# Performance work log

Hardware: AMD Instinct MI355X
Metric: run time of the kernel (lower is better)

The kernel has to match this reference:

```python
import jax, jax.numpy as jnp
from jax import lax
import numpy as np

N = 20000        # nodes
E = 160000       # directed edges (doubled to 2E inside forward)
NODE_DIM = 6
EDGE_DIM = 4
HID = 64         # hidden_dim
HEADS = 4
ITERS = 3
D_OUT = HEADS * HID          # 256
SQRT_D = 8.0                 # sqrt(HID)
ALLOWED = jnp.array([8., 23., 39., 54., 90., 180.], dtype=jnp.float32)


def _ln(x, g, b):
    m = jnp.mean(x, -1, keepdims=True)
    v = jnp.mean((x - m) ** 2, -1, keepdims=True)
    return (x - m) * lax.rsqrt(v + 1e-5) * g + b


def _cbam(x, w1, b1, w2, b2, cw, cb):
    # channel attention: pool over nodes (dim 0)
    pool = jnp.concatenate([x.max(0, keepdims=True), x.mean(0, keepdims=True)], axis=1)  # [1,2D]
    ch = jax.nn.sigmoid(jnp.maximum(pool @ w1 + b1, 0.) @ w2 + b2)                        # [1,D]
    x = x * ch
    # spatial attention: pool over features, conv1d over node axis
    cat = jnp.concatenate([x.max(-1, keepdims=True), x.mean(-1, keepdims=True)], axis=-1)  # [N,2]
    inp = cat.T[None]                                                                       # [1,2,N]
    sp = lax.conv_general_dilated(inp, cw, (1,), [(3, 3)],
                                  dimension_numbers=('NCH', 'OIH', 'NCH')) + cb[None, :, None]
    return x * jax.nn.sigmoid(sp)[0, 0][:, None]


def _tconv(xc, src, dst, wq, b_q, wk, b_k, wv, b_v, ws, b_s):
    # PyG TransformerConv (concat=True, root_weight=True, no edge features)
    n = xc.shape[0]
    q = (xc @ wq + b_q).reshape(n, HEADS, HID)
    k = (xc @ wk + b_k).reshape(n, HEADS, HID)
    v = (xc @ wv + b_v).reshape(n, HEADS, HID)
    alpha = jnp.einsum('ehd,ehd->eh', q[dst], k[src]) / SQRT_D           # [2E,H]
    amax = jax.ops.segment_max(alpha, dst, num_segments=n)
    a = jnp.exp(alpha - amax[dst])
    a = a / jax.ops.segment_sum(a, dst, num_segments=n)[dst]
    out = jax.ops.segment_sum(a[..., None] * v[src], dst, num_segments=n).reshape(n, D_OUT)
    return out + xc @ ws + b_s


def reference(x, edge_attr, node_w, node_b, edge_w, edge_b, z_emb,
              cn_w1, cn_b1, cn_w2, cn_b2, cn_cw, cn_cb,
              ce_w1, ce_b1, ce_w2, ce_b2, ce_cw, ce_cb,
              Wq, bq, Wk, bk, Wv, bv, Ws, bs,
              lt_g, lt_b, lc_g, lc_b,
              pe_w, pe_b, pn_w, pn_b, gf_w, gf_b,
              c_w1, c_b1, c_w2, c_b2, edge_index):
    send = jnp.concatenate([edge_index[0], edge_index[1]])
    recv = jnp.concatenate([edge_index[1], edge_index[0]])
    src, dst = send, recv                                           # [2E]
    rel = x[src, :3] - x[dst, :3]                                   # [2E,3]
    zi = jnp.argmin(jnp.abs(jnp.round(x[:, 2])[:, None] - ALLOWED[None, :]), axis=1)
    nf = jnp.maximum(x @ node_w + node_b, 0.) + z_emb[zi]           # node embedding + z embedding
    nf = _cbam(nf, cn_w1, cn_b1, cn_w2, cn_b2, cn_cw, cn_cb)
    ef = jnp.concatenate([jnp.concatenate([edge_attr, edge_attr], 0), rel], axis=1)
    ef = jnp.maximum(ef @ edge_w + edge_b, 0.)
    ef = _cbam(ef, ce_w1, ce_b1, ce_w2, ce_b2, ce_cw, ce_cb)
    n = nf.shape[0]
    for i in range(ITERS):
        x0, e0 = nf, ef
        agg = jax.ops.segment_sum(ef, dst, num_segments=n)          # scatter-add messages
        comb = _ln(jnp.concatenate([nf, agg - nf], 1), lc_g[i], lc_b[i])
        out = _tconv(comb, src, dst, Wq[i], bq[i], Wk[i], bk[i], Wv[i], bv[i], Ws[i], bs[i])
        out = _ln(out, lt_g[i], lt_b[i])
        pn = out @ pn_w[i] + pn_b[i]
        g = jax.nn.sigmoid(jnp.concatenate([nf, pn], 1) @ gf_w[i] + gf_b[i])  # gated fusion
        nf = nf * g + pn * (1. - g)
        ef = (out[src] - out[dst]) @ pe_w[i] + pe_b[i]
        nf = nf + x0
        ef = ef + e0
    clf = jnp.concatenate([nf[edge_index[0]], nf[edge_index[1]]], axis=1)
    h = jnp.maximum(clf @ c_w1 + c_b1, 0.)
    return (h @ c_w2 + c_b2)[:, 0]


def setup_inputs() -> dict:
    key = jax.random.key(0)
    ki = iter(jax.random.split(key, 64))
    def rn(shape, s=0.05):
        return jax.random.normal(next(ki), shape, dtype=jnp.float32) * s
    x = jax.random.normal(next(ki), (N, NODE_DIM), dtype=jnp.float32)
    x = x.at[:, 2].set(ALLOWED[jax.random.randint(next(ki), (N,), 0, 6)])
    inp = {
        'x': x,
        'edge_attr': jax.random.normal(next(ki), (E, EDGE_DIM), dtype=jnp.float32),
        'node_w': rn((NODE_DIM, HID)), 'node_b': jnp.zeros(HID),
        'edge_w': rn((EDGE_DIM + 3, HID)), 'edge_b': jnp.zeros(HID),
        'z_emb': rn((6, HID)),
        'cn_w1': rn((2 * HID, HID // 16)), 'cn_b1': jnp.zeros(HID // 16),
        'cn_w2': rn((HID // 16, HID)), 'cn_b2': jnp.zeros(HID),
        'cn_cw': rn((1, 2, 7)), 'cn_cb': jnp.zeros(1),
        'ce_w1': rn((2 * HID, HID // 16)), 'ce_b1': jnp.zeros(HID // 16),
        'ce_w2': rn((HID // 16, HID)), 'ce_b2': jnp.zeros(HID),
        'ce_cw': rn((1, 2, 7)), 'ce_cb': jnp.zeros(1),
        'Wq': rn((ITERS, 2 * HID, D_OUT)), 'bq': jnp.zeros((ITERS, D_OUT)),
        'Wk': rn((ITERS, 2 * HID, D_OUT)), 'bk': jnp.zeros((ITERS, D_OUT)),
        'Wv': rn((ITERS, 2 * HID, D_OUT)), 'bv': jnp.zeros((ITERS, D_OUT)),
        'Ws': rn((ITERS, 2 * HID, D_OUT)), 'bs': jnp.zeros((ITERS, D_OUT)),
        'lt_g': jnp.ones((ITERS, D_OUT)), 'lt_b': jnp.zeros((ITERS, D_OUT)),
        'lc_g': jnp.ones((ITERS, 2 * HID)), 'lc_b': jnp.zeros((ITERS, 2 * HID)),
        'pe_w': rn((ITERS, D_OUT, HID)), 'pe_b': jnp.zeros((ITERS, HID)),
        'pn_w': rn((ITERS, D_OUT, HID)), 'pn_b': jnp.zeros((ITERS, HID)),
        'gf_w': rn((ITERS, 2 * HID, HID)), 'gf_b': jnp.zeros((ITERS, HID)),
        'c_w1': rn((2 * HID, HID)), 'c_b1': jnp.zeros(HID),
        'c_w2': rn((HID, 1)), 'c_b2': jnp.zeros(1),
        'edge_index': jax.random.randint(next(ki), (2, E), 0, N),
    }
    return inp
```

## Files before the change

kernel.cpp:

```cpp
#include <hip/hip_runtime.h>
#include <math.h>

typedef __attribute__((ext_vector_type(8))) short short8;
typedef __attribute__((ext_vector_type(4))) float f32x4;

__device__ __forceinline__ float wave_sum(float v){
  #pragma unroll
  for (int m = 32; m; m >>= 1) v += __shfl_xor(v, m, 64);
  return v;
}
__device__ __forceinline__ float wave_max(float v){
  #pragma unroll
  for (int m = 32; m; m >>= 1) v = fmaxf(v, __shfl_xor(v, m, 64));
  return v;
}
__device__ __forceinline__ unsigned fenc(float f){
  unsigned u = __float_as_uint(f);
  return (u >> 31) ? ~u : (u | 0x80000000u);
}
__device__ __forceinline__ float fdec(unsigned e){
  return (e >> 31) ? __uint_as_float(e & 0x7fffffffu) : __uint_as_float(~e);
}
__device__ __forceinline__ float sigm(float x){ return 1.f / (1.f + __expf(-x)); }
__device__ __forceinline__ unsigned short f2bf(float f){
  union { float f; unsigned u; } x; x.f = f;
  unsigned r = x.u + 0x7fffu + ((x.u >> 16) & 1u);
  return (unsigned short)(r >> 16);
}
__device__ __forceinline__ float bf2f(unsigned short h){
  union { unsigned u; float f; } x; x.u = ((unsigned)h) << 16;
  return x.f;
}

__global__ void k_build_edges(const int* __restrict__ ei, int E2, int E,
                              int* __restrict__ src, int* __restrict__ dst,
                              int* __restrict__ deg){
  int e = blockIdx.x * blockDim.x + threadIdx.x;
  if (e >= E2) return;
  int s = ei[e];
  int d = (e < E) ? ei[e + E] : ei[e - E];
  src[e] = s; dst[e] = d;
  atomicAdd(&deg[d], 1);
}

__global__ void k_scan(const int* __restrict__ deg, int* __restrict__ rowptr, int N){
  __shared__ int part[1024];
  int t = threadIdx.x;
  int chunk = (N + 1023) / 1024;
  int lo = t * chunk, hi = lo + chunk; if (hi > N) hi = N;
  int s = 0;
  for (int i = lo; i < hi; ++i) s += deg[i];
  part[t] = s;
  __syncthreads();
  for (int off = 1; off < 1024; off <<= 1){
    int v = (t >= off) ? part[t - off] : 0;
    __syncthreads();
    part[t] += v;
    __syncthreads();
  }
  int run = part[t] - s;
  for (int i = lo; i < hi; ++i){ rowptr[i] = run; run += deg[i]; }
  if (t == 1023) rowptr[N] = part[1023];
}

__global__ void k_fill(const int* __restrict__ src, const int* __restrict__ dst,
                       const int* __restrict__ rowptr,
                       int* __restrict__ cur, int* __restrict__ csrc,
                       int* __restrict__ epos,
                       const float* __restrict__ x, const float* __restrict__ ea,
                       float* __restrict__ re8, int E2, int E){
  int e = blockIdx.x * blockDim.x + threadIdx.x;
  if (e >= E2) return;
  int s = src[e], d = dst[e];
  int pos = rowptr[d] + atomicAdd(&cur[d], 1);
  csrc[pos] = s;
  epos[e] = pos;
  int row = (e < E) ? e : e - E;
  float4 eav = *reinterpret_cast<const float4*>(ea + (size_t)row*4);
  float r0 = x[s*6]     - x[d*6];
  float r1 = x[s*6 + 1] - x[d*6 + 1];
  float r2 = x[s*6 + 2] - x[d*6 + 2];
  *reinterpret_cast<float4*>(re8 + (size_t)e*8)     = eav;
  *reinterpret_cast<float4*>(re8 + (size_t)e*8 + 4) = make_float4(r0, r1, r2, 0.f);
}

__global__ void k_embed_pool(const float* __restrict__ x, const float* __restrict__ nw,
                             const float* __restrict__ nb, const float* __restrict__ zemb,
                             float* __restrict__ nf,
                             unsigned* __restrict__ pmax, float* __restrict__ psum, int N){
  int tx = threadIdx.x & 63;
  int ty = threadIdx.x >> 6;
  const float allowed[6] = {8.f, 23.f, 39.f, 54.f, 90.f, 180.f};
  float m = -INFINITY, s = 0.f;
  for (int n = blockIdx.x*4 + ty; n < N; n += gridDim.x*4){
    float xv[6];
    #pragma unroll
    for (int k = 0; k < 6; ++k) xv[k] = x[n*6 + k];
    float v = nb[tx];
    #pragma unroll
    for (int k = 0; k < 6; ++k) v += xv[k] * nw[k*64 + tx];
    v = fmaxf(v, 0.f);
    float r = rintf(xv[2]);
    int zi = 0; float bd = fabsf(r - allowed[0]);
    #pragma unroll
    for (int k = 1; k < 6; ++k){ float d = fabsf(r - allowed[k]); if (d < bd){ bd = d; zi = k; } }
    v += zemb[zi*64 + tx];
    nf[(size_t)n*64 + tx] = v;
    m = fmaxf(m, v); s += v;
  }
  __shared__ float sm[4][64], ss[4][64];
  sm[ty][tx] = m; ss[ty][tx] = s;
  __syncthreads();
  if (ty == 0){
    #pragma unroll
    for (int k = 1; k < 4; ++k){ m = fmaxf(m, sm[k][tx]); s += ss[k][tx]; }
    atomicMax(&pmax[tx], fenc(m));
    atomicAdd(&psum[tx], s);
  }
}

__global__ void k_cbam_mlp(const unsigned* __restrict__ pmax, const float* __restrict__ psum,
                           float invR,
                           const float* __restrict__ w1, const float* __restrict__ b1,
                           const float* __restrict__ w2, const float* __restrict__ b2,
                           float* __restrict__ ch){
  __shared__ float pool[128];
  __shared__ float h[4];
  int t = threadIdx.x;
  pool[t]      = fdec(pmax[t]);
  pool[64 + t] = psum[t] * invR;
  __syncthreads();
  if (t < 4){
    float a = b1[t];
    for (int k = 0; k < 128; ++k) a += pool[k] * w1[k*4 + t];
    h[t] = fmaxf(a, 0.f);
  }
  __syncthreads();
  float a = b2[t];
  #pragma unroll
  for (int k = 0; k < 4; ++k) a += h[k] * w2[k*64 + t];
  ch[t] = sigm(a);
}

__global__ void k_chmul_rowpool(float* __restrict__ buf, const float* __restrict__ ch,
                                float* __restrict__ rp, int R){
  int r = blockIdx.x*4 + (threadIdx.x >> 6);
  if (r >= R) return;
  int l = threadIdx.x & 63;
  float v = buf[(size_t)r*64 + l] * ch[l];
  buf[(size_t)r*64 + l] = v;
  float m = wave_max(v);
  float s = wave_sum(v);
  if (l == 0){ rp[(size_t)r*2] = m; rp[(size_t)r*2 + 1] = s * (1.f/64.f); }
}

__global__ void k_spatial(float* __restrict__ buf, const float* __restrict__ rp,
                          const float* __restrict__ cw, const float* __restrict__ cb, int R){
  int r = blockIdx.x*4 + (threadIdx.x >> 6);
  if (r >= R) return;
  int l = threadIdx.x & 63;
  float sp = cb[0];
  #pragma unroll
  for (int t = 0; t < 7; ++t){
    int rr = r + t - 3;
    if (rr >= 0 && rr < R)
      sp += cw[t] * rp[(size_t)rr*2] + cw[7 + t] * rp[(size_t)rr*2 + 1];
  }
  buf[(size_t)r*64 + l] *= sigm(sp);
}

__global__ __launch_bounds__(256) void k_ecol(
    const float* __restrict__ re8,
    const float* __restrict__ ew, const float* __restrict__ eb,
    unsigned* __restrict__ pmax, float* __restrict__ psum, int E2){
  __shared__ float s_ew[448];
  __shared__ float s_re[256];
  int tid = threadIdx.x;
  for (int idx = tid; idx < 448; idx += 256) s_ew[idx] = ew[idx];
  int tx = tid & 63, wv = tid >> 6;
  float ebl = eb[tx];
  float m = -INFINITY, s = 0.f;
  for (int base = blockIdx.x*32; base < E2; base += gridDim.x*32){
    __syncthreads();
    int gidx = base*8 + tid;
    s_re[tid] = (gidx < E2*8) ? re8[gidx] : 0.f;
    __syncthreads();
    #pragma unroll
    for (int j = 0; j < 8; ++j){
      int e = base + wv*8 + j;
      if (e >= E2) break;
      const float* r = &s_re[(wv*8 + j)*8];
      float v = ebl;
      #pragma unroll
      for (int k = 0; k < 7; ++k) v += r[k] * s_ew[k*64 + tx];
      v = fmaxf(v, 0.f);
      m = fmaxf(m, v); s += v;
    }
  }
  __shared__ float sm[4][64], ss[4][64];
  sm[wv][tx] = m; ss[wv][tx] = s;
  __syncthreads();
  if (wv == 0){
    #pragma unroll
    for (int k = 1; k < 4; ++k){ m = fmaxf(m, sm[k][tx]); s += ss[k][tx]; }
    atomicMax(&pmax[tx], fenc(m));
    atomicAdd(&psum[tx], s);
  }
}

__global__ __launch_bounds__(256) void k_erp2(
    const float* __restrict__ re8, const int* __restrict__ epos,
    const float* __restrict__ ew, const float* __restrict__ eb,
    const float* __restrict__ ch,
    float* __restrict__ rp, float* __restrict__ ef0, int E2){
  __shared__ float s_ew[448];
  __shared__ float s_re[256];
  __shared__ int   s_ep[32];
  int tid = threadIdx.x;
  for (int idx = tid; idx < 448; idx += 256) s_ew[idx] = ew[idx];
  int tx = tid & 63, wv = tid >> 6;
  float ebl = eb[tx], chl = ch[tx];
  for (int base = blockIdx.x*32; base < E2; base += gridDim.x*32){
    __syncthreads();
    int gidx = base*8 + tid;
    s_re[tid] = (gidx < E2*8) ? re8[gidx] : 0.f;
    if (tid < 32 && base + tid < E2) s_ep[tid] = epos[base + tid];
    __syncthreads();
    #pragma unroll
    for (int j = 0; j < 8; ++j){
      int e = base + wv*8 + j;
      if (e >= E2) break;
      const float* r = &s_re[(wv*8 + j)*8];
      float v = ebl;
      #pragma unroll
      for (int k = 0; k < 7; ++k) v += r[k] * s_ew[k*64 + tx];
      v = fmaxf(v, 0.f) * chl;
      float mm = wave_max(v);
      float sm2 = wave_sum(v);
      if (tx == 0){ rp[(size_t)e*2] = mm; rp[(size_t)e*2 + 1] = sm2 * (1.f/64.f); }
      ef0[(size_t)s_ep[wv*8 + j]*64 + tx] = v;
    }
  }
}

__global__ void k_se(const float* __restrict__ rp, const int* __restrict__ epos,
                     const float* __restrict__ ccw, const float* __restrict__ ccb,
                     float* __restrict__ se, int E2){
  int e = blockIdx.x * blockDim.x + threadIdx.x;
  if (e >= E2) return;
  float sp = ccb[0];
  #pragma unroll
  for (int t = 0; t < 7; ++t){
    int rr = e + t - 3;
    if (rr >= 0 && rr < E2)
      sp += ccw[t] * rp[(size_t)rr*2] + ccw[7+t] * rp[(size_t)rr*2 + 1];
  }
  se[epos[e]] = sigm(sp);
}

__global__ void k_aggb(const float* __restrict__ ef0, const float* __restrict__ se,
                       const int* __restrict__ rowptr, const float* __restrict__ nf,
                       const float* __restrict__ g, const float* __restrict__ b,
                       float* __restrict__ agg, unsigned short* __restrict__ comb, int N){
  int n = blockIdx.x*4 + (threadIdx.x >> 6);
  if (n >= N) return;
  int l = threadIdx.x & 63;
  int lo = rowptr[n], hi = rowptr[n+1];
  float acc = 0.f;
  int i = lo;
  for (; i + 4 <= hi; i += 4){
    float s0 = se[i], s1 = se[i+1], s2 = se[i+2], s3 = se[i+3];
    float e0 = ef0[(size_t)i*64 + l];
    float e1 = ef0[(size_t)(i+1)*64 + l];
    float e2 = ef0[(size_t)(i+2)*64 + l];
    float e3 = ef0[(size_t)(i+3)*64 + l];
    acc += s0*e0 + s1*e1 + s2*e2 + s3*e3;
  }
  for (; i < hi; ++i) acc += se[i] * ef0[(size_t)i*64 + l];
  agg[(size_t)n*64 + l] = acc;
  float a = nf[(size_t)n*64 + l];
  float v0 = a, v1 = acc - a;
  float mean = wave_sum(v0 + v1) * (1.f/128.f);
  float d0 = v0 - mean, d1 = v1 - mean;
  float var = wave_sum(d0*d0 + d1*d1) * (1.f/128.f);
  float rs = rsqrtf(var + 1e-5f);
  comb[(size_t)n*128 + l]      = f2bf(d0 * rs * g[l]      + b[l]);
  comb[(size_t)n*128 + 64 + l] = f2bf(d1 * rs * g[64 + l] + b[64 + l]);
}

__global__ __launch_bounds__(256) void k_packT1(
    const float* __restrict__ Wq, const float* __restrict__ Wk,
    const float* __restrict__ Wv, const float* __restrict__ Ws,
    unsigned short* __restrict__ Bt){
  __shared__ float t[64][65];
  int bx = blockIdx.x, by = blockIdx.y, bz = blockIdx.z;
  const float* W = (bz == 0) ? Wq : (bz == 1) ? Wk : (bz == 2) ? Wv : Ws;
  int tx = threadIdx.x & 63, ty = threadIdx.x >> 6;
  int R0 = by*64, C0 = bx*64;
  for (int r = ty; r < 64; r += 4)
    t[r][tx] = W[(size_t)(R0 + r)*256 + C0 + tx];
  __syncthreads();
  int iter = by >> 1, kr0 = (by & 1)*64;
  for (int r = ty; r < 64; r += 4)
    Bt[(size_t)iter*1024*128 + (size_t)(bz*256 + C0 + r)*128 + kr0 + tx] = f2bf(t[tx][r]);
}

__global__ __launch_bounds__(256) void k_packT2(
    const float* __restrict__ Wn, const float* __restrict__ We,
    unsigned short* __restrict__ Bt2){
  __shared__ float t[64][65];
  int by = blockIdx.y, bz = blockIdx.z;
  const float* W = (bz == 0) ? Wn : We;
  int tx = threadIdx.x & 63, ty = threadIdx.x >> 6;
  int R0 = by*64;
  for (int r = ty; r < 64; r += 4)
    t[r][tx] = W[(size_t)(R0 + r)*64 + tx];
  __syncthreads();
  int iter = by >> 2, kr0 = (by & 3)*64;
  for (int r = ty; r < 64; r += 4)
    Bt2[(size_t)iter*128*256 + (size_t)(bz*64 + r)*256 + kr0 + tx] = f2bf(t[tx][r]);
}

__global__ void k_biasp(const float* __restrict__ bq, const float* __restrict__ bk,
                        const float* __restrict__ bv, const float* __restrict__ bs,
                        const float* __restrict__ pnb,
                        float* __restrict__ bias, float* __restrict__ bias2){
  int i = blockIdx.x, t = threadIdx.x;
  const float* bb = (t < 256) ? bq : (t < 512) ? bk : (t < 768) ? bv : bs;
  bias[i*1024 + t] = bb[i*256 + (t & 255)];
  if (t < 64)       bias2[i*128 + t] = pnb[i*64 + t];
  else if (t < 128) bias2[i*128 + t] = 0.f;
}

__global__ void k_packC(const float* __restrict__ cw1, float* __restrict__ Wp){
  int idx = blockIdx.x * blockDim.x + threadIdx.x;
  if (idx >= 64*128) return;
  int k = idx >> 7, j = idx & 127;
  Wp[idx] = (j < 64) ? cw1[k*64 + j] : cw1[(64 + k)*64 + (j - 64)];
}

template<int NSTEPS, int MODE>
__global__ __launch_bounds__(256) void k_mfma(
    const unsigned short* __restrict__ A, int lda,
    const unsigned short* __restrict__ Bt, int ldb,
    const float* __restrict__ bias,
    float* __restrict__ o_f0, unsigned short* __restrict__ o_h0,
    unsigned short* __restrict__ o_h1, float* __restrict__ o_f1, int M){
  __shared__ char lds[65536];
  char* ldsA = lds;
  char* ldsB = lds + 32768;
  int tid = threadIdx.x;
  int nbase = blockIdx.x * 128;
  int mbase = blockIdx.y * 128;
  int l = tid & 63, wid = tid >> 6;
  int wm = (wid >> 1) * 64, wn = (wid & 1) * 64;
  f32x4 acc[4][4] = {};
  const char* Ab  = (const char*)A;
  const char* Btb = (const char*)Bt;
  for (int ks = 0; ks < NSTEPS; ++ks){
    #pragma unroll
    for (int it = 0; it < 8; ++it){
      int c = tid + it*256;
      int row = c >> 4;
      int kb = (c & 15) << 4;
      int off = (row << 8) + (kb ^ ((row & 7) << 4));
      uint4 va = make_uint4(0,0,0,0);
      int gr = mbase + row;
      if (gr < M)
        va = *reinterpret_cast<const uint4*>(Ab + (size_t)gr*(lda*2) + ks*256 + kb);
      *reinterpret_cast<uint4*>(ldsA + off) = va;
      uint4 vb = *reinterpret_cast<const uint4*>(
                   Btb + (size_t)(nbase + row)*(ldb*2) + ks*256 + kb);
      *reinterpret_cast<uint4*>(ldsB + off) = vb;
    }
    __syncthreads();
    #pragma unroll
    for (int kk = 0; kk < 4; ++kk){
      int kbyte = kk*64 + (l >> 4)*16;
      short8 af[4], bf[4];
      #pragma unroll
      for (int m = 0; m < 4; ++m){
        int fr = wm + m*16 + (l & 15);
        af[m] = *reinterpret_cast<const short8*>(ldsA + (fr << 8) + (kbyte ^ ((fr & 7) << 4)));
      }
      #pragma unroll
      for (int n = 0; n < 4; ++n){
        int fc = wn + n*16 + (l & 15);
        bf[n] = *reinterpret_cast<const short8*>(ldsB + (fc << 8) + (kbyte ^ ((fc & 7) << 4)));
      }
      #pragma unroll
      for (int m = 0; m < 4; ++m)
        #pragma unroll
        for (int n = 0; n < 4; ++n)
          acc[m][n] = __builtin_amdgcn_mfma_f32_16x16x32_bf16(af[m], bf[n], acc[m][n], 0, 0, 0);
    }
    __syncthreads();
  }
  #pragma unroll
  for (int n = 0; n < 4; ++n){
    int gcol = nbase + wn + n*16 + (l & 15);
    float bv = bias ? bias[gcol] : 0.f;
    #pragma unroll
    for (int m = 0; m < 4; ++m){
      int grow = mbase + wm + m*16 + (l >> 4)*4;
      #pragma unroll
      for (int r = 0; r < 4; ++r){
        int gr = grow + r;
        if (gr < M){
          float val = acc[m][n][r] + bv;
          if (MODE == 1){
            o_f0[(size_t)gr*128 + gcol] = val;
          } else {
            int seg = gcol >> 8, c = gcol & 255;
            if      (seg == 0) o_f0[(size_t)gr*256 + c] = val;
            else if (seg == 1) o_h0[(size_t)gr*256 + c] = f2bf(val);
            else if (seg == 2) o_h1[(size_t)gr*256 + c] = f2bf(val);
            else               o_f1[(size_t)gr*256 + c] = val;
          }
        }
      }
    }
  }
}

__global__ void k_attn(const float* __restrict__ q, const unsigned short* __restrict__ kbuf,
                       const unsigned short* __restrict__ vbuf, const float* __restrict__ sbuf,
                       const int* __restrict__ rowptr, const int* __restrict__ csrc,
                       const float* __restrict__ ltg, const float* __restrict__ ltb,
                       unsigned short* __restrict__ outb, int N){
  int n = blockIdx.x*4 + (threadIdx.x >> 6);
  if (n >= N) return;
  int l = threadIdx.x & 63;
  int lo = rowptr[n], hi = rowptr[n+1];
  size_t base = (size_t)n*256 + l*4;
  const int l4 = l*4;
  float4 qv = *reinterpret_cast<const float4*>(q + base);
  qv.x *= 0.125f; qv.y *= 0.125f; qv.z *= 0.125f; qv.w *= 0.125f;
  float o0 = 0.f, o1 = 0.f, o2 = 0.f, o3 = 0.f, s = 0.f;
  int i = lo;
  for (; i + 8 <= hi; i += 8){
    ushort4 kk[8], vv[8];
    #pragma unroll
    for (int j = 0; j < 8; ++j){
      int c = csrc[i + j];
      kk[j] = *reinterpret_cast<const ushort4*>(kbuf + (size_t)c*256 + l4);
      vv[j] = *reinterpret_cast<const ushort4*>(vbuf + (size_t)c*256 + l4);
    }
    float a[8];
    #pragma unroll
    for (int j = 0; j < 8; ++j)
      a[j] = qv.x*bf2f(kk[j].x) + qv.y*bf2f(kk[j].y) + qv.z*bf2f(kk[j].z) + qv.w*bf2f(kk[j].w);
    #pragma unroll
    for (int m = 1; m < 16; m <<= 1){
      #pragma unroll
      for (int j = 0; j < 8; ++j) a[j] += __shfl_xor(a[j], m, 64);
    }
    #pragma unroll
    for (int j = 0; j < 8; ++j){
      float w = __expf(a[j]);
      s += w;
      o0 += w*bf2f(vv[j].x); o1 += w*bf2f(vv[j].y);
      o2 += w*bf2f(vv[j].z); o3 += w*bf2f(vv[j].w);
    }
  }
  for (; i < hi; ++i){
    size_t sb = (size_t)csrc[i]*256 + l4;
    ushort4 kv = *reinterpret_cast<const ushort4*>(kbuf + sb);
    ushort4 vv = *reinterpret_cast<const ushort4*>(vbuf + sb);
    float a = qv.x*bf2f(kv.x) + qv.y*bf2f(kv.y) + qv.z*bf2f(kv.z) + qv.w*bf2f(kv.w);
    #pragma unroll
    for (int m = 1; m < 16; m <<= 1) a += __shfl_xor(a, m, 64);
    float w = __expf(a);
    s += w;
    o0 += w*bf2f(vv.x); o1 += w*bf2f(vv.y); o2 += w*bf2f(vv.z); o3 += w*bf2f(vv.w);
  }
  float4 t = *reinterpret_cast<const float4*>(sbuf + base);
  if (hi > lo){
    float r = 1.f / s;
    t.x += o0*r; t.y += o1*r; t.z += o2*r; t.w += o3*r;
  }
  float mean = wave_sum(t.x + t.y + t.z + t.w) * (1.f/256.f);
  float dx = t.x - mean, dy = t.y - mean, dz = t.z - mean, dw = t.w - mean;
  float var = wave_sum(dx*dx + dy*dy + dz*dz + dw*dw) * (1.f/256.f);
  float rs = rsqrtf(var + 1e-5f);
  float4 g = *reinterpret_cast<const float4*>(ltg + l4);
  float4 b = *reinterpret_cast<const float4*>(ltb + l4);
  ushort4 o;
  o.x = f2bf(dx*rs*g.x + b.x);
  o.y = f2bf(dy*rs*g.y + b.y);
  o.z = f2bf(dz*rs*g.z + b.z);
  o.w = f2bf(dw*rs*g.w + b.w);
  *reinterpret_cast<ushort4*>(outb + base) = o;
}

__global__ __launch_bounds__(256) void k_gate_agg(
    float* __restrict__ nf, float* __restrict__ agg,
    const float* __restrict__ pnP,
    const int* __restrict__ rowptr, const int* __restrict__ csrc,
    const float* __restrict__ gfw, const float* __restrict__ gfb,
    const float* __restrict__ peb,
    const float* __restrict__ cg, const float* __restrict__ cbv,
    unsigned short* __restrict__ comb, int doComb, int N){
  __shared__ float s_w[128 * 64];
  int tid = threadIdx.x;
  for (int idx = tid; idx < 128*64; idx += 256) s_w[idx] = gfw[idx];
  __syncthreads();
  int wv = tid >> 6, l = tid & 63;
  float gb = gfb[l], pebl = peb[l];
  for (int n = blockIdx.x*4 + wv; n < N; n += gridDim.x*4){
    float nfv = nf[(size_t)n*64 + l];
    float pnv = pnP[(size_t)n*128 + l];
    float g = gb;
    #pragma unroll 8
    for (int k = 0; k < 64; ++k){
      g += __shfl(nfv, k, 64) * s_w[k*64 + l];
      g += __shfl(pnv, k, 64) * s_w[(64 + k)*64 + l];
    }
    g = sigm(g);
    float nfn = nfv * (1.f + g) + pnv * (1.f - g);
    nf[(size_t)n*64 + l] = nfn;
    int lo = rowptr[n], hi = rowptr[n+1];
    float sp = 0.f;
    int i = lo;
    for (; i + 8 <= hi; i += 8){
      float pv[8];
      #pragma unroll
      for (int j = 0; j < 8; ++j)
        pv[j] = pnP[(size_t)csrc[i+j]*128 + 64 + l];
      #pragma unroll
      for (int j = 0; j < 8; ++j) sp += pv[j];
    }
    for (; i < hi; ++i) sp += pnP[(size_t)csrc[i]*128 + 64 + l];
    float Pn = pnP[(size_t)n*128 + 64 + l];
    float aggn = agg[(size_t)n*64 + l] + sp - (float)(hi - lo) * (Pn - pebl);
    agg[(size_t)n*64 + l] = aggn;
    if (doComb){
      float v0 = nfn, v1 = aggn - nfn;
      float mean = wave_sum(v0 + v1) * (1.f/128.f);
      float d0 = v0 - mean, d1 = v1 - mean;
      float var = wave_sum(d0*d0 + d1*d1) * (1.f/128.f);
      float rs = rsqrtf(var + 1e-5f);
      comb[(size_t)n*128 + l]      = f2bf(d0 * rs * cg[l]      + cbv[l]);
      comb[(size_t)n*128 + 64 + l] = f2bf(d1 * rs * cg[64 + l] + cbv[64 + l]);
    }
  }
}

template<int K, int BN>
__global__ __launch_bounds__(256) void k_gemm(
    const float* __restrict__ in, const float* __restrict__ W, int ldw,
    const float* __restrict__ bias, float* __restrict__ out, int ldo, int nrows){
  constexpr int PAD = BN + 4;
  __shared__ float s_in[K * PAD];
  int n0 = blockIdx.x * BN;
  int tid = threadIdx.x;
  for (int idx = tid; idx < BN * K; idx += 256){
    int r = idx / K, k = idx - r * K;
    float v = (n0 + r < nrows) ? in[(size_t)(n0 + r) * K + k] : 0.f;
    s_in[k * PAD + r] = v;
  }
  __syncthreads();
  int tx = tid & 15, ty = tid >> 4;
  constexpr int NT = BN / 16;
  int col0 = blockIdx.y * 64 + tx * 4;
  float acc[NT][4] = {};
  for (int k = 0; k < K; ++k){
    const float4 wv = *reinterpret_cast<const float4*>(&W[(size_t)k * ldw + col0]);
    #pragma unroll
    for (int i = 0; i < NT; ++i){
      float cv = s_in[k * PAD + ty * NT + i];
      acc[i][0] += cv * wv.x;
      acc[i][1] += cv * wv.y;
      acc[i][2] += cv * wv.z;
      acc[i][3] += cv * wv.w;
    }
  }
  #pragma unroll
  for (int i = 0; i < NT; ++i){
    int n = n0 + ty * NT + i;
    if (n < nrows){
      float4 o = make_float4(acc[i][0], acc[i][1], acc[i][2], acc[i][3]);
      *reinterpret_cast<float4*>(&out[(size_t)n * ldo + col0]) = o;
    }
  }
}

__global__ void k_final(const float* __restrict__ AB,
                        const int* __restrict__ ei, const float* __restrict__ cb1,
                        const float* __restrict__ cw2, const float* __restrict__ cb2,
                        float* __restrict__ dout, int E){
  int e = blockIdx.x*4 + (threadIdx.x >> 6);
  if (e >= E) return;
  int l = threadIdx.x & 63;
  int i0 = ei[e], i1 = ei[E + e];
  float h = fmaxf(AB[(size_t)i0*128 + l] + AB[(size_t)i1*128 + 64 + l] + cb1[l], 0.f);
  float p = wave_sum(h * cw2[l]);
  if (l == 0) dout[e] = p + cb2[0];
}

extern "C" void kernel_launch(void* const* d_in, const int* in_sizes, int n_in,
                              void* d_out, int out_size, void* d_ws, size_t ws_size,
                              hipStream_t stream){
  const float* x         = (const float*)d_in[0];
  const float* edge_attr = (const float*)d_in[1];
  const float* node_w    = (const float*)d_in[2];
  const float* node_b    = (const float*)d_in[3];
  const float* edge_w    = (const float*)d_in[4];
  const float* edge_b    = (const float*)d_in[5];
  const float* z_emb     = (const float*)d_in[6];
  const float* cn_w1     = (const float*)d_in[7];
  const float* cn_b1     = (const float*)d_in[8];
  const float* cn_w2     = (const float*)d_in[9];
  const float* cn_b2     = (const float*)d_in[10];
  const float* cn_cw     = (const float*)d_in[11];
  const float* cn_cb     = (const float*)d_in[12];
  const float* ce_w1     = (const float*)d_in[13];
  const float* ce_b1     = (const float*)d_in[14];
  const float* ce_w2     = (const float*)d_in[15];
  const float* ce_b2     = (const float*)d_in[16];
  const float* ce_cw     = (const float*)d_in[17];
  const float* ce_cb     = (const float*)d_in[18];
  const float* Wq        = (const float*)d_in[19];
  const float* bq        = (const float*)d_in[20];
  const float* Wk        = (const float*)d_in[21];
  const float* bk        = (const float*)d_in[22];
  const float* Wv        = (const float*)d_in[23];
  const float* bv        = (const float*)d_in[24];
  const float* Ws        = (const float*)d_in[25];
  const float* bs        = (const float*)d_in[26];
  const float* lt_g      = (const float*)d_in[27];
  const float* lt_b      = (const float*)d_in[28];
  const float* lc_g      = (const float*)d_in[29];
  const float* lc_b      = (const float*)d_in[30];
  const float* pe_w      = (const float*)d_in[31];
  const float* pe_b      = (const float*)d_in[32];
  const float* pn_w      = (const float*)d_in[33];
  const float* pn_b      = (const float*)d_in[34];
  const float* gf_w      = (const float*)d_in[35];
  const float* gf_b      = (const float*)d_in[36];
  const float* c_w1      = (const float*)d_in[37];
  const float* c_b1      = (const float*)d_in[38];
  const float* c_w2      = (const float*)d_in[39];
  const float* c_b2      = (const float*)d_in[40];
  const int*   edge_index= (const int*)d_in[41];

  const int N  = in_sizes[0] / 6;
  const int E  = in_sizes[1] / 4;
  const int E2 = 2 * E;

  char* p = (char*)d_ws;
  auto alloc = [&](size_t bytes)->char*{
    char* r = p; p += (bytes + 255) & ~(size_t)255; return r;
  };
  int*            w_src    = (int*)           alloc((size_t)E2 * 4);
  int*            w_dst    = (int*)           alloc((size_t)E2 * 4);
  int*            w_deg    = (int*)           alloc((size_t)N * 4);
  int*            w_rowptr = (int*)           alloc((size_t)(N + 1) * 4);
  int*            w_cur    = (int*)           alloc((size_t)N * 4);
  int*            w_csrc   = (int*)           alloc((size_t)E2 * 4);
  int*            w_epos   = (int*)           alloc((size_t)E2 * 4);
  float*          w_re8    = (float*)         alloc((size_t)E2 * 8 * 4);
  float*          w_nf     = (float*)         alloc((size_t)N * 64 * 4);
  float*          w_agg    = (float*)         alloc((size_t)N * 64 * 4);
  float*          w_ef0    = (float*)         alloc((size_t)E2 * 64 * 4);
  float*          w_se     = (float*)         alloc((size_t)E2 * 4);
  unsigned short* w_comb   = (unsigned short*)alloc((size_t)N * 128 * 2);
  float*          w_q      = (float*)         alloc((size_t)N * 256 * 4);
  unsigned short* w_k      = (unsigned short*)alloc((size_t)N * 256 * 2);
  unsigned short* w_v      = (unsigned short*)alloc((size_t)N * 256 * 2);
  float*          w_s      = (float*)         alloc((size_t)N * 256 * 4);
  unsigned short* w_outb   = (unsigned short*)alloc((size_t)N * 256 * 2);
  float*          w_pnP    = (float*)         alloc((size_t)N * 128 * 4);
  float*          w_rp     = (float*)         alloc((size_t)E2 * 2 * 4);
  float*          w_AB     = (float*)         alloc((size_t)N * 128 * 4);
  float*          w_Wp     = (float*)         alloc((size_t)64 * 128 * 4);
  unsigned short* w_Bt     = (unsigned short*)alloc((size_t)3 * 1024 * 128 * 2);
  float*          w_bias   = (float*)         alloc((size_t)3 * 1024 * 4);
  unsigned short* w_Bt2    = (unsigned short*)alloc((size_t)3 * 128 * 256 * 2);
  float*          w_bias2  = (float*)         alloc((size_t)3 * 128 * 4);
  unsigned*       w_pmax   = (unsigned*)      alloc(64 * 4);
  float*          w_psum   = (float*)         alloc(64 * 4);
  float*          w_ch     = (float*)         alloc(64 * 4);
  unsigned*       w_pmax2  = (unsigned*)      alloc(64 * 4);
  float*          w_psum2  = (float*)         alloc(64 * 4);
  float*          w_ch2    = (float*)         alloc(64 * 4);

  hipMemsetAsync(w_deg,  0, (size_t)N * 4, stream);
  hipMemsetAsync(w_cur,  0, (size_t)N * 4, stream);
  hipMemsetAsync(w_pmax, 0, 64 * 4, stream);
  hipMemsetAsync(w_psum, 0, 64 * 4, stream);
  hipMemsetAsync(w_pmax2,0, 64 * 4, stream);
  hipMemsetAsync(w_psum2,0, 64 * 4, stream);

  k_build_edges<<<(E2 + 255)/256, 256, 0, stream>>>(edge_index, E2, E, w_src, w_dst, w_deg);
  k_scan<<<1, 1024, 0, stream>>>(w_deg, w_rowptr, N);
  k_fill<<<(E2 + 255)/256, 256, 0, stream>>>(w_src, w_dst, w_rowptr, w_cur, w_csrc, w_epos,
                                             x, edge_attr, w_re8, E2, E);
  k_embed_pool<<<512, 256, 0, stream>>>(x, node_w, node_b, z_emb, w_nf, w_pmax, w_psum, N);
  k_cbam_mlp<<<1, 64, 0, stream>>>(w_pmax, w_psum, 1.f/(float)N,
                                   cn_w1, cn_b1, cn_w2, cn_b2, w_ch);
  k_chmul_rowpool<<<(N + 3)/4, 256, 0, stream>>>(w_nf, w_ch, w_rp, N);
  k_spatial<<<(N + 3)/4, 256, 0, stream>>>(w_nf, w_rp, cn_cw, cn_cb, N);

  k_ecol<<<2048, 256, 0, stream>>>(w_re8, edge_w, edge_b, w_pmax2, w_psum2, E2);
  k_cbam_mlp<<<1, 64, 0, stream>>>(w_pmax2, w_psum2, 1.f/(float)E2,
                                   ce_w1, ce_b1, ce_w2, ce_b2, w_ch2);
  k_erp2<<<2048, 256, 0, stream>>>(w_re8, w_epos, edge_w, edge_b, w_ch2,
                                   w_rp, w_ef0, E2);
  k_se<<<(E2 + 255)/256, 256, 0, stream>>>(w_rp, w_epos, ce_cw, ce_cb, w_se, E2);
  k_aggb<<<(N + 3)/4, 256, 0, stream>>>(w_ef0, w_se, w_rowptr, w_nf,
                                        lc_g, lc_b, w_agg, w_comb, N);

  k_packT1<<<dim3(4, 6, 4), 256, 0, stream>>>(Wq, Wk, Wv, Ws, w_Bt);
  k_packT2<<<dim3(1, 12, 2), 256, 0, stream>>>(pn_w, pe_w, w_Bt2);
  k_biasp<<<3, 1024, 0, stream>>>(bq, bk, bv, bs, pn_b, w_bias, w_bias2);
  k_packC<<<32, 256, 0, stream>>>(c_w1, w_Wp);

  const int MB = (N + 127) / 128;
  for (int i = 0; i < 3; ++i){
    k_mfma<1,0><<<dim3(8, MB), 256, 0, stream>>>(w_comb, 128,
                                                 w_Bt + (size_t)i*1024*128, 128,
                                                 w_bias + (size_t)i*1024,
                                                 w_q, w_k, w_v, w_s, N);
    k_attn<<<(N + 3)/4, 256, 0, stream>>>(w_q, w_k, w_v, w_s, w_rowptr, w_csrc,
                                          lt_g + (size_t)i*256, lt_b + (size_t)i*256,
                                          w_outb, N);
    k_mfma<2,1><<<dim3(1, MB), 256, 0, stream>>>(w_outb, 256,
                                                 w_Bt2 + (size_t)i*128*256, 256,
                                                 w_bias2 + (size_t)i*128,
                                                 w_pnP, nullptr, nullptr, nullptr, N);
    int doComb = (i < 2) ? 1 : 0;
    const float* cg  = lc_g + (size_t)(i < 2 ? i+1 : 0)*128;
    const float* cbv = lc_b + (size_t)(i < 2 ? i+1 : 0)*128;
    k_gate_agg<<<1250, 256, 0, stream>>>(w_nf, w_agg, w_pnP, w_rowptr, w_csrc,
                                         gf_w + (size_t)i*128*64, gf_b + (size_t)i*64,
                                         pe_b + (size_t)i*64,
                                         cg, cbv, w_comb, doComb, N);
  }

  dim3 gAB((N + 63)/64, 2);
  k_gemm<64,64><<<gAB, 256, 0, stream>>>(w_nf, w_Wp, 128, nullptr, w_AB, 128, N);
  k_final<<<(E + 3)/4, 256, 0, stream>>>(w_AB, edge_index, c_b1, c_w2, c_b2,
                                         (float*)d_out, E);
}
```

Before: 857.7 us.

## Move gate linear layer from scalar shuffle loop to bf16 MFMA GEMM

The per-node gate projection [nf, pn] @ gf_w used to be computed inside k_gate_agg with wave shuffles and LDS weights. It is now an MFMA GEMM over a bf16 input buffer (gin), which k_spatial, the pn GEMM epilogue and k_gate2 fill in. A new packing kernel transposes gf_w to bf16 with zero-padded columns. The intent is to replace about 128 shuffle-FMAs per element with matrix-core work. The cost is one extra launch per iteration, extra global traffic for gin and the gate buffer, bf16 rounding of the gate inputs, and half of the GEMM columns being wasted padding.

```diff
diff --git a/kernel.cpp b/kernel.cpp
--- a/kernel.cpp
+++ b/kernel.cpp
@@ -155,7 +155,8 @@
 }
 
 __global__ void k_spatial(float* __restrict__ buf, const float* __restrict__ rp,
-                          const float* __restrict__ cw, const float* __restrict__ cb, int R){
+                          const float* __restrict__ cw, const float* __restrict__ cb,
+                          unsigned short* __restrict__ gin, int R){
   int r = blockIdx.x*4 + (threadIdx.x >> 6);
   if (r >= R) return;
   int l = threadIdx.x & 63;
@@ -166,7 +167,9 @@
     if (rr >= 0 && rr < R)
       sp += cw[t] * rp[(size_t)rr*2] + cw[7 + t] * rp[(size_t)rr*2 + 1];
   }
-  buf[(size_t)r*64 + l] *= sigm(sp);
+  float v = buf[(size_t)r*64 + l] * sigm(sp);
+  buf[(size_t)r*64 + l] = v;
+  gin[(size_t)r*128 + l] = f2bf(v);
 }
 
 __global__ __launch_bounds__(256) void k_ecol(
@@ -321,15 +324,30 @@
     Bt2[(size_t)iter*128*256 + (size_t)(bz*64 + r)*256 + kr0 + tx] = f2bf(t[tx][r]);
 }
 
+__global__ void k_packG(const float* __restrict__ gfw, unsigned short* __restrict__ BtG){
+  int b = blockIdx.x;
+  int iter = b >> 7, col = b & 127;
+  int k = threadIdx.x;
+  unsigned short v = 0;
+  if (col < 64) v = f2bf(gfw[(size_t)iter*128*64 + (size_t)k*64 + col]);
+  BtG[(size_t)b*128 + k] = v;
+}
+
 __global__ void k_biasp(const float* __restrict__ bq, const float* __restrict__ bk,
                         const float* __restrict__ bv, const float* __restrict__ bs,
-                        const float* __restrict__ pnb,
-                        float* __restrict__ bias, float* __restrict__ bias2){
+                        const float* __restrict__ pnb, const float* __restrict__ gfb,
+                        float* __restrict__ bias, float* __restrict__ bias2,
+                        float* __restrict__ bias3){
   int i = blockIdx.x, t = threadIdx.x;
   const float* bb = (t < 256) ? bq : (t < 512) ? bk : (t < 768) ? bv : bs;
   bias[i*1024 + t] = bb[i*256 + (t & 255)];
-  if (t < 64)       bias2[i*128 + t] = pnb[i*64 + t];
-  else if (t < 128) bias2[i*128 + t] = 0.f;
+  if (t < 64){
+    bias2[i*128 + t] = pnb[i*64 + t];
+    bias3[i*128 + t] = gfb[i*64 + t];
+  } else if (t < 128){
+    bias2[i*128 + t] = 0.f;
+    bias3[i*128 + t] = 0.f;
+  }
 }
 
 __global__ void k_packC(const float* __restrict__ cw1, float* __restrict__ Wp){
@@ -410,6 +428,9 @@
           float val = acc[m][n][r] + bv;
           if (MODE == 1){
             o_f0[(size_t)gr*128 + gcol] = val;
+            if (gcol < 64) o_h0[(size_t)gr*128 + 64 + gcol] = f2bf(val);
+          } else if (MODE == 2){
+            if (gcol < 64) o_f0[(size_t)gr*64 + gcol] = val;
           } else {
             int seg = gcol >> 8, c = gcol & 255;
             if      (seg == 0) o_f0[(size_t)gr*256 + c] = val;
@@ -493,56 +514,46 @@
   *reinterpret_cast<ushort4*>(outb + base) = o;
 }
 
-__global__ __launch_bounds__(256) void k_gate_agg(
+__global__ __launch_bounds__(256) void k_gate2(
     float* __restrict__ nf, float* __restrict__ agg,
-    const float* __restrict__ pnP,
+    const float* __restrict__ pnP, const float* __restrict__ gate_arg,
     const int* __restrict__ rowptr, const int* __restrict__ csrc,
-    const float* __restrict__ gfw, const float* __restrict__ gfb,
     const float* __restrict__ peb,
     const float* __restrict__ cg, const float* __restrict__ cbv,
-    unsigned short* __restrict__ comb, int doComb, int N){
-  __shared__ float s_w[128 * 64];
-  int tid = threadIdx.x;
-  for (int idx = tid; idx < 128*64; idx += 256) s_w[idx] = gfw[idx];
-  __syncthreads();
-  int wv = tid >> 6, l = tid & 63;
-  float gb = gfb[l], pebl = peb[l];
-  for (int n = blockIdx.x*4 + wv; n < N; n += gridDim.x*4){
-    float nfv = nf[(size_t)n*64 + l];
-    float pnv = pnP[(size_t)n*128 + l];
-    float g = gb;
-    #pragma unroll 8
-    for (int k = 0; k < 64; ++k){
-      g += __shfl(nfv, k, 64) * s_w[k*64 + l];
-      g += __shfl(pnv, k, 64) * s_w[(64 + k)*64 + l];
-    }
-    g = sigm(g);
-    float nfn = nfv * (1.f + g) + pnv * (1.f - g);
-    nf[(size_t)n*64 + l] = nfn;
-    int lo = rowptr[n], hi = rowptr[n+1];
-    float sp = 0.f;
-    int i = lo;
-    for (; i + 8 <= hi; i += 8){
-      float pv[8];
-      #pragma unroll
-      for (int j = 0; j < 8; ++j)
-        pv[j] = pnP[(size_t)csrc[i+j]*128 + 64 + l];
-      #pragma unroll
-      for (int j = 0; j < 8; ++j) sp += pv[j];
-    }
-    for (; i < hi; ++i) sp += pnP[(size_t)csrc[i]*128 + 64 + l];
-    float Pn = pnP[(size_t)n*128 + 64 + l];
-    float aggn = agg[(size_t)n*64 + l] + sp - (float)(hi - lo) * (Pn - pebl);
-    agg[(size_t)n*64 + l] = aggn;
-    if (doComb){
-      float v0 = nfn, v1 = aggn - nfn;
-      float mean = wave_sum(v0 + v1) * (1.f/128.f);
-      float d0 = v0 - mean, d1 = v1 - mean;
-      float var = wave_sum(d0*d0 + d1*d1) * (1.f/128.f);
-      float rs = rsqrtf(var + 1e-5f);
-      comb[(size_t)n*128 + l]      = f2bf(d0 * rs * cg[l]      + cbv[l]);
-      comb[(size_t)n*128 + 64 + l] = f2bf(d1 * rs * cg[64 + l] + cbv[64 + l]);
-    }
+    unsigned short* __restrict__ comb, unsigned short* __restrict__ gin,
+    int doComb, int N){
+  int n = blockIdx.x*4 + (threadIdx.x >> 6);
+  if (n >= N) return;
+  int l = threadIdx.x & 63;
+  float g = sigm(gate_arg[(size_t)n*64 + l]);
+  float nfv = nf[(size_t)n*64 + l];
+  float pnv = pnP[(size_t)n*128 + l];
+  float nfn = nfv * (1.f + g) + pnv * (1.f - g);
+  nf[(size_t)n*64 + l] = nfn;
+  gin[(size_t)n*128 + l] = f2bf(nfn);
+  int lo = rowptr[n], hi = rowptr[n+1];
+  float sp = 0.f;
+  int i = lo;
+  for (; i + 8 <= hi; i += 8){
+    float pv[8];
+    #pragma unroll
+    for (int j = 0; j < 8; ++j)
+      pv[j] = pnP[(size_t)csrc[i+j]*128 + 64 + l];
+    #pragma unroll
+    for (int j = 0; j < 8; ++j) sp += pv[j];
+  }
+  for (; i < hi; ++i) sp += pnP[(size_t)csrc[i]*128 + 64 + l];
+  float Pn = pnP[(size_t)n*128 + 64 + l];
+  float aggn = agg[(size_t)n*64 + l] + sp - (float)(hi - lo) * (Pn - peb[l]);
+  agg[(size_t)n*64 + l] = aggn;
+  if (doComb){
+    float v0 = nfn, v1 = aggn - nfn;
+    float mean = wave_sum(v0 + v1) * (1.f/128.f);
+    float d0 = v0 - mean, d1 = v1 - mean;
+    float var = wave_sum(d0*d0 + d1*d1) * (1.f/128.f);
+    float rs = rsqrtf(var + 1e-5f);
+    comb[(size_t)n*128 + l]      = f2bf(d0 * rs * cg[l]      + cbv[l]);
+    comb[(size_t)n*128 + 64 + l] = f2bf(d1 * rs * cg[64 + l] + cbv[64 + l]);
   }
 }
 
@@ -665,6 +676,8 @@
   float*          w_ef0    = (float*)         alloc((size_t)E2 * 64 * 4);
   float*          w_se     = (float*)         alloc((size_t)E2 * 4);
   unsigned short* w_comb   = (unsigned short*)alloc((size_t)N * 128 * 2);
+  unsigned short* w_gin    = (unsigned short*)alloc((size_t)N * 128 * 2);
+  float*          w_gate   = (float*)         alloc((size_t)N * 64 * 4);
   float*          w_q      = (float*)         alloc((size_t)N * 256 * 4);
   unsigned short* w_k      = (unsigned short*)alloc((size_t)N * 256 * 2);
   unsigned short* w_v      = (unsigned short*)alloc((size_t)N * 256 * 2);
@@ -678,6 +691,8 @@
   float*          w_bias   = (float*)         alloc((size_t)3 * 1024 * 4);
   unsigned short* w_Bt2    = (unsigned short*)alloc((size_t)3 * 128 * 256 * 2);
   float*          w_bias2  = (float*)         alloc((size_t)3 * 128 * 4);
+  unsigned short* w_BtG    = (unsigned short*)alloc((size_t)3 * 128 * 128 * 2);
+  float*          w_bias3  = (float*)         alloc((size_t)3 * 128 * 4);
   unsigned*       w_pmax   = (unsigned*)      alloc(64 * 4);
   float*          w_psum   = (float*)         alloc(64 * 4);
   float*          w_ch     = (float*)         alloc(64 * 4);
@@ -700,7 +715,7 @@
   k_cbam_mlp<<<1, 64, 0, stream>>>(w_pmax, w_psum, 1.f/(float)N,
                                    cn_w1, cn_b1, cn_w2, cn_b2, w_ch);
   k_chmul_rowpool<<<(N + 3)/4, 256, 0, stream>>>(w_nf, w_ch, w_rp, N);
-  k_spatial<<<(N + 3)/4, 256, 0, stream>>>(w_nf, w_rp, cn_cw, cn_cb, N);
+  k_spatial<<<(N + 3)/4, 256, 0, stream>>>(w_nf, w_rp, cn_cw, cn_cb, w_gin, N);
 
   k_ecol<<<2048, 256, 0, stream>>>(w_re8, edge_w, edge_b, w_pmax2, w_psum2, E2);
   k_cbam_mlp<<<1, 64, 0, stream>>>(w_pmax2, w_psum2, 1.f/(float)E2,
@@ -713,7 +728,8 @@
 
   k_packT1<<<dim3(4, 6, 4), 256, 0, stream>>>(Wq, Wk, Wv, Ws, w_Bt);
   k_packT2<<<dim3(1, 12, 2), 256, 0, stream>>>(pn_w, pe_w, w_Bt2);
-  k_biasp<<<3, 1024, 0, stream>>>(bq, bk, bv, bs, pn_b, w_bias, w_bias2);
+  k_packG<<<3*128, 128, 0, stream>>>(gf_w, w_BtG);
+  k_biasp<<<3, 1024, 0, stream>>>(bq, bk, bv, bs, pn_b, gf_b, w_bias, w_bias2, w_bias3);
   k_packC<<<32, 256, 0, stream>>>(c_w1, w_Wp);
 
   const int MB = (N + 127) / 128;
@@ -728,14 +744,18 @@
     k_mfma<2,1><<<dim3(1, MB), 256, 0, stream>>>(w_outb, 256,
                                                  w_Bt2 + (size_t)i*128*256, 256,
                                                  w_bias2 + (size_t)i*128,
-                                                 w_pnP, nullptr, nullptr, nullptr, N);
+                                                 w_pnP, w_gin, nullptr, nullptr, N);
+    k_mfma<1,2><<<dim3(1, MB), 256, 0, stream>>>(w_gin, 128,
+                                                 w_BtG + (size_t)i*128*128, 128,
+                                                 w_bias3 + (size_t)i*128,
+                                                 w_gate, nullptr, nullptr, nullptr, N);
     int doComb = (i < 2) ? 1 : 0;
     const float* cg  = lc_g + (size_t)(i < 2 ? i+1 : 0)*128;
     const float* cbv = lc_b + (size_t)(i < 2 ? i+1 : 0)*128;
-    k_gate_agg<<<1250, 256, 0, stream>>>(w_nf, w_agg, w_pnP, w_rowptr, w_csrc,
-                                         gf_w + (size_t)i*128*64, gf_b + (size_t)i*64,
-                                         pe_b + (size_t)i*64,
-                                         cg, cbv, w_comb, doComb, N);
+    k_gate2<<<(N + 3)/4, 256, 0, stream>>>(w_nf, w_agg, w_pnP, w_gate,
+                                           w_rowptr, w_csrc,
+                                           pe_b + (size_t)i*64,
+                                           cg, cbv, w_comb, w_gin, doComb, N);
   }
 
   dim3 gAB((N + 63)/64, 2);
```

After: 786.9 us. 8.2% less time.
